# Optimization experiments

Hardware: AMD Instinct MI355X
Metric: run time of the kernel (lower is better)

## Reference

```python
import jax, jax.numpy as jnp
import numpy as np

B, E, N, M = 2, 512, 4096, 4096

def setup_inputs() -> dict:
    key = jax.random.key(0)
    ks = jax.random.split(key, 8)
    s = 1.0 / np.sqrt(E)
    return {
        "src_embedding": jax.random.normal(ks[0], (B, E, N), jnp.float32),
        "tgt_embedding": jax.random.normal(ks[1], (B, E, M), jnp.float32),
        "src": jax.random.normal(ks[2], (B, 3, N), jnp.float32),
        "tgt": jax.random.normal(ks[3], (B, 3, M), jnp.float32),
        "Wq": jax.random.normal(ks[4], (E, E), jnp.float32) * s,
        "bq": jax.random.normal(ks[5], (E,), jnp.float32) * s,
        "Wk": jax.random.normal(ks[6], (E, E), jnp.float32) * s,
        "bk": jax.random.normal(ks[7], (E,), jnp.float32) * s,
    }

def reference(src_embedding, tgt_embedding, src, tgt, Wq, bq, Wk, bk):
    # query/key: [B, N, E] after transpose + Linear (y = x @ W^T + b)
    q = jnp.einsum('ben,fe->bnf', src_embedding, Wq) + bq
    k = jnp.einsum('bem,fe->bmf', tgt_embedding, Wk) + bk
    # pairwise_distance[b,n,m] = -||q_n||^2 + 2 q_n.k_m - ||k_m||^2 = -||q_n - k_m||^2
    inner = jnp.einsum('bne,bme->bnm', q, k)          # [B, N, M]
    qq = jnp.sum(q * q, axis=-1)                      # [B, N]
    kk = jnp.sum(k * k, axis=-1)                      # [B, M]
    pairwise = 2.0 * inner - qq[:, :, None] - kk[:, None, :]
    scores = jax.nn.softmax(pairwise, axis=2)         # softmax over keys (M)
    # src_corr = tgt @ scores^T : [B, 3, N]
    src_corr = jnp.einsum('bdm,bnm->bdn', tgt, scores)
    return (src, src_corr)
```

## Files before the change

kernel.cpp:

```cpp
#include <hip/hip_runtime.h>


typedef _Float16 f16;
typedef __attribute__((ext_vector_type(8))) _Float16 f16x8;
typedef __attribute__((ext_vector_type(4))) float f32x4;

constexpr int B_ = 2, E_ = 512, N_ = 4096, M_ = 4096;
constexpr int MCH = 8;
constexpr float WSCALE = 64.0f;

__device__ __forceinline__ f32x4 mfma16(f16x8 a, f16x8 b, f32x4 c) {
  return __builtin_amdgcn_mfma_f32_16x16x32_f16(a, b, c, 0, 0, 0);
}

__device__ __forceinline__ void gll16(const void* g, void* l) {
  __builtin_amdgcn_global_load_lds(
      (const __attribute__((address_space(1))) unsigned int*)g,
      (__attribute__((address_space(3))) unsigned int*)l, 16, 0, 0);
}


__device__ __forceinline__ void gemm_hl22(
    const f16* __restrict__ AH, const f16* __restrict__ AL,
    const f16* __restrict__ BH, const f16* __restrict__ BL,
    char* lds, f32x4 (&acc)[4][4])
{
  char* ldsA = lds;
  char* ldsB = lds + 16384;
  const int l = threadIdx.x & 63, w = threadIdx.x >> 6;
  const int q = (l & 7) ^ (l >> 3);
  const int rA = w * 8 + (l >> 3);
  const size_t srcoff = (size_t)rA * E_ + (q & 3) * 8;
  const f16* sA = (q < 4 ? AH : AL) + srcoff;
  const f16* sB = (q < 4 ? BH : BL) + srcoff;
  char* dA = ldsA + w * 1024;
  char* dB = ldsB + w * 1024;

  const int r15 = l & 15;
  const int pH16 = ((l >> 4) ^ (l & 7)) * 16;
  const int wr = (w >> 1) * 64, wc = (w & 1) * 64;
  const char* rAh = ldsA + (wr + r15) * 128 + pH16;
  const char* rAl = ldsA + (wr + r15) * 128 + (pH16 ^ 64);
  const char* rBh = ldsB + (wc + r15) * 128 + pH16;
  const char* rBl = ldsB + (wc + r15) * 128 + (pH16 ^ 64);

  for (int e0 = 0; e0 < E_; e0 += 32) {
#pragma unroll
    for (int c = 0; c < 4; ++c) {
      gll16(sA + (size_t)c * 32 * E_, dA + c * 4096);
      gll16(sB + (size_t)c * 32 * E_, dB + c * 4096);
    }
    sA += 32; sB += 32;
    __syncthreads();
    f16x8 ah[4], al[4], bh[4], bl[4];
#pragma unroll
    for (int i = 0; i < 4; ++i) {
      ah[i] = *(const f16x8*)(rAh + i * 2048);
      al[i] = *(const f16x8*)(rAl + i * 2048);
      bh[i] = *(const f16x8*)(rBh + i * 2048);
      bl[i] = *(const f16x8*)(rBl + i * 2048);
    }
#pragma unroll
    for (int i = 0; i < 4; ++i)
#pragma unroll
      for (int j = 0; j < 4; ++j) {
        acc[i][j] = mfma16(ah[i], bh[j], acc[i][j]);
        acc[i][j] = mfma16(ah[i], bl[j], acc[i][j]);
        acc[i][j] = mfma16(al[i], bh[j], acc[i][j]);
      }
    __syncthreads();
  }
}

__device__ __forceinline__ void gemm_hl41(
    const f16* __restrict__ AH, const f16* __restrict__ AL,
    const f16* __restrict__ BH, const f16* __restrict__ BL,
    char* lds, f32x4 (&acc)[2][8])
{
  char* ldsA = lds;
  char* ldsB = lds + 16384;
  const int l = threadIdx.x & 63, w = threadIdx.x >> 6;
  const int q = (l & 7) ^ (l >> 3);
  const int rA = w * 8 + (l >> 3);
  const size_t srcoff = (size_t)rA * E_ + (q & 3) * 8;
  const f16* sA = (q < 4 ? AH : AL) + srcoff;
  const f16* sB = (q < 4 ? BH : BL) + srcoff;
  char* dA = ldsA + w * 1024;
  char* dB = ldsB + w * 1024;

  const int r15 = l & 15;
  const int pH16 = ((l >> 4) ^ (l & 7)) * 16;
  const char* rAh = ldsA + (w * 32 + r15) * 128 + pH16;
  const char* rAl = ldsA + (w * 32 + r15) * 128 + (pH16 ^ 64);
  const char* rBh = ldsB + r15 * 128 + pH16;
  const char* rBl = ldsB + r15 * 128 + (pH16 ^ 64);

  for (int e0 = 0; e0 < E_; e0 += 32) {
#pragma unroll
    for (int c = 0; c < 4; ++c) {
      gll16(sA + (size_t)c * 32 * E_, dA + c * 4096);
      gll16(sB + (size_t)c * 32 * E_, dB + c * 4096);
    }
    sA += 32; sB += 32;
    __syncthreads();
    f16x8 ah0 = *(const f16x8*)(rAh);
    f16x8 ah1 = *(const f16x8*)(rAh + 2048);
    f16x8 al0 = *(const f16x8*)(rAl);
    f16x8 al1 = *(const f16x8*)(rAl + 2048);
#pragma unroll
    for (int j = 0; j < 8; ++j) {
      f16x8 bh = *(const f16x8*)(rBh + j * 2048);
      f16x8 bl = *(const f16x8*)(rBl + j * 2048);
      acc[0][j] = mfma16(ah0, bh, acc[0][j]);
      acc[1][j] = mfma16(ah1, bh, acc[1][j]);
      acc[0][j] = mfma16(ah0, bl, acc[0][j]);
      acc[1][j] = mfma16(ah1, bl, acc[1][j]);
      acc[0][j] = mfma16(al0, bh, acc[0][j]);
      acc[1][j] = mfma16(al1, bh, acc[1][j]);
    }
    __syncthreads();
  }
}

__global__ void k_split_w(const float* __restrict__ Wq, const float* __restrict__ Wk,
                          f16* __restrict__ WqH, f16* __restrict__ WqL,
                          f16* __restrict__ WkH, f16* __restrict__ WkL) {
  int i = blockIdx.x * 256 + threadIdx.x;
  float a = Wq[i] * WSCALE;
  f16 ah = (f16)a; WqH[i] = ah; WqL[i] = (f16)(a - (float)ah);
  float b = Wk[i] * WSCALE;
  f16 bh = (f16)b; WkH[i] = bh; WkL[i] = (f16)(b - (float)bh);
}

__global__ void k_tsplit(const float* __restrict__ Xq, const float* __restrict__ Xk,
                         f16* __restrict__ XqH, f16* __restrict__ XqL,
                         f16* __restrict__ XkH, f16* __restrict__ XkL) {
  __shared__ float tile[64][65];
  const int b = blockIdx.z >> 1, which = blockIdx.z & 1;
  const float* X = (which ? Xk : Xq) + (size_t)b * E_ * N_;
  f16* H = (which ? XkH : XqH) + (size_t)b * N_ * E_;
  f16* L = (which ? XkL : XqL) + (size_t)b * N_ * E_;
  const int e0 = blockIdx.x * 64, n0 = blockIdx.y * 64;
  const int x = threadIdx.x, y = threadIdx.y;
#pragma unroll
  for (int j = 0; j < 16; ++j) {
    int e = y * 16 + j;
    tile[e][x] = X[(size_t)(e0 + e) * N_ + n0 + x];
  }
  __syncthreads();
#pragma unroll
  for (int j = 0; j < 16; ++j) {
    int nl = y * 16 + j;
    float v = tile[x][nl];
    f16 h = (f16)v;
    H[(size_t)(n0 + nl) * E_ + e0 + x] = h;
    L[(size_t)(n0 + nl) * E_ + e0 + x] = (f16)(v - (float)h);
  }
}

__global__ __launch_bounds__(256) void k_proj(
    const f16* __restrict__ XqH, const f16* __restrict__ XqL,
    const f16* __restrict__ XkH, const f16* __restrict__ XkL,
    const f16* __restrict__ WqH, const f16* __restrict__ WqL,
    const f16* __restrict__ WkH, const f16* __restrict__ WkL,
    const float* __restrict__ bq, const float* __restrict__ bk,
    f16* __restrict__ QH, f16* __restrict__ QL,
    f16* __restrict__ KH, f16* __restrict__ KL) {
  __shared__ char lds[32768];
  const int b = blockIdx.z >> 1, kind = blockIdx.z & 1;
  const f16* AH = (kind ? XkH : XqH) + (size_t)b * N_ * E_;
  const f16* AL = (kind ? XkL : XqL) + (size_t)b * N_ * E_;
  const f16* BH = kind ? WkH : WqH;
  const f16* BL = kind ? WkL : WqL;
  const float* bias = kind ? bk : bq;
  f16* OH = (kind ? KH : QH) + (size_t)b * N_ * E_;
  f16* OL = (kind ? KL : QL) + (size_t)b * N_ * E_;
  const int n0 = blockIdx.x * 128, f0 = blockIdx.y * 128;
  const int lane = threadIdx.x & 63, w = threadIdx.x >> 6;
  const int wr = (w >> 1) * 64, wc = (w & 1) * 64;
  const int r15 = lane & 15;

  f32x4 acc[4][4] = {};
  gemm_hl22(AH + (size_t)n0 * E_, AL + (size_t)n0 * E_,
            BH + (size_t)f0 * E_, BL + (size_t)f0 * E_, lds, acc);

  const int rowg = (lane >> 4) * 4;
#pragma unroll
  for (int j = 0; j < 4; ++j) {
    int f = f0 + wc + j * 16 + r15;
    float bv = bias[f];
#pragma unroll
    for (int i = 0; i < 4; ++i) {
#pragma unroll
      for (int r = 0; r < 4; ++r) {
        int n = n0 + wr + i * 16 + rowg + r;
        float qv = acc[i][j][r] * (1.0f / WSCALE) + bv;
        f16 h = (f16)qv;
        OH[(size_t)n * E_ + f] = h;
        OL[(size_t)n * E_ + f] = (f16)(qv - (float)h);
      }
    }
  }
}

__global__ void k_kk(const f16* __restrict__ KH, const f16* __restrict__ KL,
                     float* __restrict__ kk) {
  int row = blockIdx.x * 4 + (threadIdx.x >> 6);
  int lane = threadIdx.x & 63;
  f16x8 h8 = *(const f16x8*)(KH + (size_t)row * E_ + lane * 8);
  f16x8 l8 = *(const f16x8*)(KL + (size_t)row * E_ + lane * 8);
  float s = 0.f;
#pragma unroll
  for (int i = 0; i < 8; ++i) {
    float v = (float)h8[i] + (float)l8[i];
    s += v * v;
  }
#pragma unroll
  for (int o = 32; o; o >>= 1) s += __shfl_xor(s, o);
  if (lane == 0) kk[row] = s;
}

__global__ __launch_bounds__(256, 2) void k_flash(
    const f16* __restrict__ QH, const f16* __restrict__ QL,
    const f16* __restrict__ KH, const f16* __restrict__ KL,
    const float* __restrict__ kk, const float* __restrict__ tgt,
    float* __restrict__ part) {
  __shared__ char lds[40960];
  float* kks = (float*)(lds + 32768);
  float* tgs = (float*)(lds + 34816);
  const int b = blockIdx.z;
  const int n0 = blockIdx.x * 128;
  const int mc = blockIdx.y;
  const int m0c = mc * 512;
  const int tid = threadIdx.x, l = tid & 63, w = tid >> 6;
  const int r15 = l & 15;

  for (int i = tid; i < 512; i += 256) kks[i] = kk[(size_t)b * M_ + m0c + i];
  for (int i = tid; i < 1536; i += 256) {
    int d = i >> 9, m = i & 511;
    tgs[i] = tgt[((size_t)b * 3 + d) * M_ + m0c + m];
  }

  const f16* AH = QH + ((size_t)b * N_ + n0) * E_;
  const f16* AL = QL + ((size_t)b * N_ + n0) * E_;

  float mrun[8], psum[8], pp0[8], pp1[8], pp2[8];
#pragma unroll
  for (int x = 0; x < 8; ++x) {
    mrun[x] = -3.0e38f; psum[x] = 0.f; pp0[x] = 0.f; pp1[x] = 0.f; pp2[x] = 0.f;
  }

  for (int mt = 0; mt < 4; ++mt) {
    const int m0 = m0c + mt * 128;
    const f16* BH = KH + ((size_t)b * M_ + m0) * E_;
    const f16* BL = KL + ((size_t)b * M_ + m0) * E_;
    f32x4 acc[2][8] = {};
    gemm_hl41(AH, AL, BH, BL, lds, acc);

    float kv[8], tv0[8], tv1[8], tv2[8];
#pragma unroll
    for (int j = 0; j < 8; ++j) {
      int ml = mt * 128 + j * 16 + r15;
      kv[j] = kks[ml];
      tv0[j] = tgs[ml];
      tv1[j] = tgs[512 + ml];
      tv2[j] = tgs[1024 + ml];
    }
#pragma unroll
    for (int i = 0; i < 2; ++i) {
#pragma unroll
      for (int r = 0; r < 4; ++r) {
        const int x = i * 4 + r;
        float s[8];
        float rmax = -3.0e38f;
#pragma unroll
        for (int j = 0; j < 8; ++j) {
          s[j] = 2.0f * acc[i][j][r] - kv[j];
          rmax = fmaxf(rmax, s[j]);
        }
        rmax = fmaxf(rmax, __shfl_xor(rmax, 1));
        rmax = fmaxf(rmax, __shfl_xor(rmax, 2));
        rmax = fmaxf(rmax, __shfl_xor(rmax, 4));
        rmax = fmaxf(rmax, __shfl_xor(rmax, 8));
        float nm = fmaxf(mrun[x], rmax);
        float sc = __expf(mrun[x] - nm);
        mrun[x] = nm;
        psum[x] *= sc; pp0[x] *= sc; pp1[x] *= sc; pp2[x] *= sc;
#pragma unroll
        for (int j = 0; j < 8; ++j) {
          float e = __expf(s[j] - nm);
          psum[x] += e;
          pp0[x] += e * tv0[j];
          pp1[x] += e * tv1[j];
          pp2[x] += e * tv2[j];
        }
      }
    }
  }

#pragma unroll
  for (int x = 0; x < 8; ++x) {
#pragma unroll
    for (int o = 1; o <= 8; o <<= 1) {
      psum[x] += __shfl_xor(psum[x], o);
      pp0[x] += __shfl_xor(pp0[x], o);
      pp1[x] += __shfl_xor(pp1[x], o);
      pp2[x] += __shfl_xor(pp2[x], o);
    }
  }
  if (r15 == 0) {
    const int hi = l >> 4;
#pragma unroll
    for (int x = 0; x < 8; ++x) {
      int i = x >> 2, r = x & 3;
      int n = n0 + w * 32 + i * 16 + hi * 4 + r;
      size_t pb = ((size_t)(b * N_ + n) * MCH + mc) * 5;
      part[pb + 0] = mrun[x];
      part[pb + 1] = psum[x];
      part[pb + 2] = pp0[x];
      part[pb + 3] = pp1[x];
      part[pb + 4] = pp2[x];
    }
  }
}

__global__ void k_comb(const float* __restrict__ part, float* __restrict__ out) {
  int idx = blockIdx.x * 256 + threadIdx.x;
  int b = idx >> 12, n = idx & (N_ - 1);
  const float* p = part + (size_t)idx * MCH * 5;
  float M = -3.0e38f;
#pragma unroll
  for (int c = 0; c < MCH; ++c) M = fmaxf(M, p[c * 5]);
  float S = 0.f, P0 = 0.f, P1 = 0.f, P2 = 0.f;
#pragma unroll
  for (int c = 0; c < MCH; ++c) {
    float e = __expf(p[c * 5] - M);
    S += p[c * 5 + 1] * e;
    P0 += p[c * 5 + 2] * e;
    P1 += p[c * 5 + 3] * e;
    P2 += p[c * 5 + 4] * e;
  }
  float inv = 1.0f / S;
  float* oc = out + (size_t)B_ * 3 * N_;
  oc[((size_t)b * 3 + 0) * N_ + n] = P0 * inv;
  oc[((size_t)b * 3 + 1) * N_ + n] = P1 * inv;
  oc[((size_t)b * 3 + 2) * N_ + n] = P2 * inv;
}

__global__ void k_copy(const float* __restrict__ src, float* __restrict__ out) {
  int i = blockIdx.x * 256 + threadIdx.x;
  out[i] = src[i];
}

extern "C" void kernel_launch(void* const* d_in, const int* in_sizes, int n_in,
                              void* d_out, int out_size, void* d_ws, size_t ws_size,
                              hipStream_t stream) {
  const float* src_emb = (const float*)d_in[0];
  const float* tgt_emb = (const float*)d_in[1];
  const float* src     = (const float*)d_in[2];
  const float* tgt     = (const float*)d_in[3];
  const float* Wq      = (const float*)d_in[4];
  const float* bq      = (const float*)d_in[5];
  const float* Wk      = (const float*)d_in[6];
  const float* bk      = (const float*)d_in[7];
  float* out = (float*)d_out;

  constexpr size_t SZX = (size_t)B_ * N_ * E_;
  constexpr size_t OFFW = 4 * SZX * sizeof(f16);
  constexpr size_t OFFQ = OFFW + 4 * (size_t)E_ * E_ * sizeof(f16);
  constexpr size_t OFFK2 = OFFQ + 4 * SZX * sizeof(f16);
  constexpr size_t OFFP = OFFK2 + (size_t)B_ * M_ * sizeof(float);
  constexpr size_t NEED = OFFP + (size_t)B_ * N_ * MCH * 5 * sizeof(float);
  if (ws_size < NEED) return;

  char* ws = (char*)d_ws;
  f16* XqH = (f16*)(ws);
  f16* XqL = XqH + SZX;
  f16* XkH = XqL + SZX;
  f16* XkL = XkH + SZX;
  f16* WqH = (f16*)(ws + OFFW);
  f16* WqL = WqH + (size_t)E_ * E_;
  f16* WkH = WqL + (size_t)E_ * E_;
  f16* WkL = WkH + (size_t)E_ * E_;
  f16* QH = (f16*)(ws + OFFQ);
  f16* QL = QH + SZX;
  f16* KH = QL + SZX;
  f16* KL = KH + SZX;
  float* kk = (float*)(ws + OFFK2);
  float* part = (float*)(ws + OFFP);

  k_split_w<<<dim3(E_ * E_ / 256), 256, 0, stream>>>(Wq, Wk, WqH, WqL, WkH, WkL);
  k_tsplit<<<dim3(E_ / 64, N_ / 64, B_ * 2), dim3(64, 4), 0, stream>>>(
      src_emb, tgt_emb, XqH, XqL, XkH, XkL);
  k_proj<<<dim3(N_ / 128, E_ / 128, B_ * 2), 256, 0, stream>>>(
      XqH, XqL, XkH, XkL, WqH, WqL, WkH, WkL, bq, bk, QH, QL, KH, KL);
  k_kk<<<dim3(B_ * M_ / 4), 256, 0, stream>>>(KH, KL, kk);
  k_flash<<<dim3(N_ / 128, MCH, B_), 256, 0, stream>>>(QH, QL, KH, KL, kk, tgt, part);
  k_comb<<<dim3(B_ * N_ / 256), 256, 0, stream>>>(part, out);
  k_copy<<<dim3(B_ * 3 * N_ / 256), 256, 0, stream>>>(src, out);
}
```

Before: 250.1 us.

## Double-buffer LDS tiles with async prefetch in projection and flash GEMMs

Replaces the single-buffered GEMM helpers with inline double-buffered loops. The next K-slice is issued via global_load_lds while the current one is consumed, with vmcnt waits and raw s_barrier in place of __syncthreads. In the flash kernel the prefetch runs continuously across the M-tile boundaries. It also adds setprio around the MFMA blocks and raises launch bounds for k_proj. LDS use doubles (64KB and 72KB per block), which may limit occupancy. The flash kernel's 72KB may not allow two blocks per CU as its launch bounds request.

```diff
diff --git a/kernel.cpp b/kernel.cpp
--- a/kernel.cpp
+++ b/kernel.cpp
@@ -12,115 +12,14 @@
 __device__ __forceinline__ f32x4 mfma16(f16x8 a, f16x8 b, f32x4 c) {
   return __builtin_amdgcn_mfma_f32_16x16x32_f16(a, b, c, 0, 0, 0);
 }
-
 __device__ __forceinline__ void gll16(const void* g, void* l) {
   __builtin_amdgcn_global_load_lds(
       (const __attribute__((address_space(1))) unsigned int*)g,
       (__attribute__((address_space(3))) unsigned int*)l, 16, 0, 0);
 }
-
-
-__device__ __forceinline__ void gemm_hl22(
-    const f16* __restrict__ AH, const f16* __restrict__ AL,
-    const f16* __restrict__ BH, const f16* __restrict__ BL,
-    char* lds, f32x4 (&acc)[4][4])
-{
-  char* ldsA = lds;
-  char* ldsB = lds + 16384;
-  const int l = threadIdx.x & 63, w = threadIdx.x >> 6;
-  const int q = (l & 7) ^ (l >> 3);
-  const int rA = w * 8 + (l >> 3);
-  const size_t srcoff = (size_t)rA * E_ + (q & 3) * 8;
-  const f16* sA = (q < 4 ? AH : AL) + srcoff;
-  const f16* sB = (q < 4 ? BH : BL) + srcoff;
-  char* dA = ldsA + w * 1024;
-  char* dB = ldsB + w * 1024;
-
-  const int r15 = l & 15;
-  const int pH16 = ((l >> 4) ^ (l & 7)) * 16;
-  const int wr = (w >> 1) * 64, wc = (w & 1) * 64;
-  const char* rAh = ldsA + (wr + r15) * 128 + pH16;
-  const char* rAl = ldsA + (wr + r15) * 128 + (pH16 ^ 64);
-  const char* rBh = ldsB + (wc + r15) * 128 + pH16;
-  const char* rBl = ldsB + (wc + r15) * 128 + (pH16 ^ 64);
-
-  for (int e0 = 0; e0 < E_; e0 += 32) {
-#pragma unroll
-    for (int c = 0; c < 4; ++c) {
-      gll16(sA + (size_t)c * 32 * E_, dA + c * 4096);
-      gll16(sB + (size_t)c * 32 * E_, dB + c * 4096);
-    }
-    sA += 32; sB += 32;
-    __syncthreads();
-    f16x8 ah[4], al[4], bh[4], bl[4];
-#pragma unroll
-    for (int i = 0; i < 4; ++i) {
-      ah[i] = *(const f16x8*)(rAh + i * 2048);
-      al[i] = *(const f16x8*)(rAl + i * 2048);
-      bh[i] = *(const f16x8*)(rBh + i * 2048);
-      bl[i] = *(const f16x8*)(rBl + i * 2048);
-    }
-#pragma unroll
-    for (int i = 0; i < 4; ++i)
-#pragma unroll
-      for (int j = 0; j < 4; ++j) {
-        acc[i][j] = mfma16(ah[i], bh[j], acc[i][j]);
-        acc[i][j] = mfma16(ah[i], bl[j], acc[i][j]);
-        acc[i][j] = mfma16(al[i], bh[j], acc[i][j]);
-      }
-    __syncthreads();
-  }
-}
-
-__device__ __forceinline__ void gemm_hl41(
-    const f16* __restrict__ AH, const f16* __restrict__ AL,
-    const f16* __restrict__ BH, const f16* __restrict__ BL,
-    char* lds, f32x4 (&acc)[2][8])
-{
-  char* ldsA = lds;
-  char* ldsB = lds + 16384;
-  const int l = threadIdx.x & 63, w = threadIdx.x >> 6;
-  const int q = (l & 7) ^ (l >> 3);
-  const int rA = w * 8 + (l >> 3);
-  const size_t srcoff = (size_t)rA * E_ + (q & 3) * 8;
-  const f16* sA = (q < 4 ? AH : AL) + srcoff;
-  const f16* sB = (q < 4 ? BH : BL) + srcoff;
-  char* dA = ldsA + w * 1024;
-  char* dB = ldsB + w * 1024;
-
-  const int r15 = l & 15;
-  const int pH16 = ((l >> 4) ^ (l & 7)) * 16;
-  const char* rAh = ldsA + (w * 32 + r15) * 128 + pH16;
-  const char* rAl = ldsA + (w * 32 + r15) * 128 + (pH16 ^ 64);
-  const char* rBh = ldsB + r15 * 128 + pH16;
-  const char* rBl = ldsB + r15 * 128 + (pH16 ^ 64);
-
-  for (int e0 = 0; e0 < E_; e0 += 32) {
-#pragma unroll
-    for (int c = 0; c < 4; ++c) {
-      gll16(sA + (size_t)c * 32 * E_, dA + c * 4096);
-      gll16(sB + (size_t)c * 32 * E_, dB + c * 4096);
-    }
-    sA += 32; sB += 32;
-    __syncthreads();
-    f16x8 ah0 = *(const f16x8*)(rAh);
-    f16x8 ah1 = *(const f16x8*)(rAh + 2048);
-    f16x8 al0 = *(const f16x8*)(rAl);
-    f16x8 al1 = *(const f16x8*)(rAl + 2048);
-#pragma unroll
-    for (int j = 0; j < 8; ++j) {
-      f16x8 bh = *(const f16x8*)(rBh + j * 2048);
-      f16x8 bl = *(const f16x8*)(rBl + j * 2048);
-      acc[0][j] = mfma16(ah0, bh, acc[0][j]);
-      acc[1][j] = mfma16(ah1, bh, acc[1][j]);
-      acc[0][j] = mfma16(ah0, bl, acc[0][j]);
-      acc[1][j] = mfma16(ah1, bl, acc[1][j]);
-      acc[0][j] = mfma16(al0, bh, acc[0][j]);
-      acc[1][j] = mfma16(al1, bh, acc[1][j]);
-    }
-    __syncthreads();
-  }
-}
+__device__ __forceinline__ void waitv8() { asm volatile("s_waitcnt vmcnt(8)" ::: "memory"); }
+__device__ __forceinline__ void waitv0() { asm volatile("s_waitcnt vmcnt(0)" ::: "memory"); }
+
 
 __global__ void k_split_w(const float* __restrict__ Wq, const float* __restrict__ Wk,
                           f16* __restrict__ WqH, f16* __restrict__ WqL,
@@ -158,7 +57,7 @@
   }
 }
 
-__global__ __launch_bounds__(256) void k_proj(
+__global__ __launch_bounds__(256, 2) void k_proj(
     const f16* __restrict__ XqH, const f16* __restrict__ XqL,
     const f16* __restrict__ XkH, const f16* __restrict__ XkL,
     const f16* __restrict__ WqH, const f16* __restrict__ WqL,
@@ -166,7 +65,7 @@
     const float* __restrict__ bq, const float* __restrict__ bk,
     f16* __restrict__ QH, f16* __restrict__ QL,
     f16* __restrict__ KH, f16* __restrict__ KL) {
-  __shared__ char lds[32768];
+  __shared__ char lds[65536];
   const int b = blockIdx.z >> 1, kind = blockIdx.z & 1;
   const f16* AH = (kind ? XkH : XqH) + (size_t)b * N_ * E_;
   const f16* AL = (kind ? XkL : XqL) + (size_t)b * N_ * E_;
@@ -176,15 +75,62 @@
   f16* OH = (kind ? KH : QH) + (size_t)b * N_ * E_;
   f16* OL = (kind ? KL : QL) + (size_t)b * N_ * E_;
   const int n0 = blockIdx.x * 128, f0 = blockIdx.y * 128;
-  const int lane = threadIdx.x & 63, w = threadIdx.x >> 6;
+  const int l = threadIdx.x & 63, w = threadIdx.x >> 6;
   const int wr = (w >> 1) * 64, wc = (w & 1) * 64;
-  const int r15 = lane & 15;
+  const int r15 = l & 15;
+
+  const int q = (l & 7) ^ (l >> 3);
+  const size_t soff = (size_t)(w * 8 + (l >> 3)) * E_ + (q & 3) * 8;
+  const f16* sA = (q < 4 ? AH : AL) + (size_t)n0 * E_ + soff;
+  const f16* sB = (q < 4 ? BH : BL) + (size_t)f0 * E_ + soff;
+
+  auto STAGE = [&](int k) {
+    char* dA = lds + ((k & 1) << 14) + w * 1024;
+    char* dB = lds + 32768 + ((k & 1) << 14) + w * 1024;
+    const f16* pa = sA + k * 32;
+    const f16* pb = sB + k * 32;
+#pragma unroll
+    for (int c = 0; c < 4; ++c) {
+      gll16(pa + (size_t)c * 32 * E_, dA + c * 4096);
+      gll16(pb + (size_t)c * 32 * E_, dB + c * 4096);
+    }
+  };
+
+  const int pH16 = ((l >> 4) ^ (l & 7)) * 16;
+  const int aoffH = (wr + r15) * 128 + pH16;
+  const int boffH = (wc + r15) * 128 + pH16;
 
   f32x4 acc[4][4] = {};
-  gemm_hl22(AH + (size_t)n0 * E_, AL + (size_t)n0 * E_,
-            BH + (size_t)f0 * E_, BL + (size_t)f0 * E_, lds, acc);
-
-  const int rowg = (lane >> 4) * 4;
+  STAGE(0);
+#pragma unroll 2
+  for (int k = 0; k < 16; ++k) {
+    if (k < 15) { STAGE(k + 1); waitv8(); } else { waitv0(); }
+    __builtin_amdgcn_sched_barrier(0);
+    __builtin_amdgcn_s_barrier();
+    const char* cA = lds + ((k & 1) << 14);
+    const char* cB = lds + 32768 + ((k & 1) << 14);
+    f16x8 ah[4], al[4], bh[4], bl[4];
+#pragma unroll
+    for (int i = 0; i < 4; ++i) {
+      ah[i] = *(const f16x8*)(cA + aoffH + i * 2048);
+      al[i] = *(const f16x8*)(cA + (aoffH ^ 64) + i * 2048);
+      bh[i] = *(const f16x8*)(cB + boffH + i * 2048);
+      bl[i] = *(const f16x8*)(cB + (boffH ^ 64) + i * 2048);
+    }
+    __builtin_amdgcn_s_setprio(1);
+#pragma unroll
+    for (int i = 0; i < 4; ++i)
+#pragma unroll
+      for (int j = 0; j < 4; ++j) {
+        acc[i][j] = mfma16(ah[i], bh[j], acc[i][j]);
+        acc[i][j] = mfma16(ah[i], bl[j], acc[i][j]);
+        acc[i][j] = mfma16(al[i], bh[j], acc[i][j]);
+      }
+    __builtin_amdgcn_s_setprio(0);
+    __builtin_amdgcn_s_barrier();
+  }
+
+  const int rowg = (l >> 4) * 4;
 #pragma unroll
   for (int j = 0; j < 4; ++j) {
     int f = f0 + wc + j * 16 + r15;
@@ -225,13 +171,12 @@
     const f16* __restrict__ KH, const f16* __restrict__ KL,
     const float* __restrict__ kk, const float* __restrict__ tgt,
     float* __restrict__ part) {
-  __shared__ char lds[40960];
-  float* kks = (float*)(lds + 32768);
-  float* tgs = (float*)(lds + 34816);
+  __shared__ char lds[73728];
+  float* kks = (float*)(lds + 65536);
+  float* tgs = (float*)(lds + 67584);
   const int b = blockIdx.z;
   const int n0 = blockIdx.x * 128;
-  const int mc = blockIdx.y;
-  const int m0c = mc * 512;
+  const int mc = blockIdx.y, m0c = mc * 512;
   const int tid = threadIdx.x, l = tid & 63, w = tid >> 6;
   const int r15 = l & 15;
 
@@ -243,6 +188,30 @@
 
   const f16* AH = QH + ((size_t)b * N_ + n0) * E_;
   const f16* AL = QL + ((size_t)b * N_ + n0) * E_;
+  const f16* BHb = KH + ((size_t)b * M_ + m0c) * E_;
+  const f16* BLb = KL + ((size_t)b * M_ + m0c) * E_;
+
+  const int q = (l & 7) ^ (l >> 3);
+  const size_t soff = (size_t)(w * 8 + (l >> 3)) * E_ + (q & 3) * 8;
+  const f16* sA = (q < 4 ? AH : AL) + soff;
+  const f16* sB = (q < 4 ? BHb : BLb) + soff;
+
+  auto STAGE = [&](int s) {
+    int mt_ = s >> 4, k_ = s & 15;
+    char* dA = lds + ((s & 1) << 14) + w * 1024;
+    char* dB = lds + 32768 + ((s & 1) << 14) + w * 1024;
+    const f16* pa = sA + k_ * 32;
+    const f16* pb = sB + (size_t)mt_ * 128 * E_ + k_ * 32;
+#pragma unroll
+    for (int c = 0; c < 4; ++c) {
+      gll16(pa + (size_t)c * 32 * E_, dA + c * 4096);
+      gll16(pb + (size_t)c * 32 * E_, dB + c * 4096);
+    }
+  };
+
+  const int pH16 = ((l >> 4) ^ (l & 7)) * 16;
+  const int aoffH = (w * 32 + r15) * 128 + pH16;
+  const int boffH = r15 * 128 + pH16;
 
   float mrun[8], psum[8], pp0[8], pp1[8], pp2[8];
 #pragma unroll
@@ -250,12 +219,36 @@
     mrun[x] = -3.0e38f; psum[x] = 0.f; pp0[x] = 0.f; pp1[x] = 0.f; pp2[x] = 0.f;
   }
 
+  STAGE(0);
   for (int mt = 0; mt < 4; ++mt) {
-    const int m0 = m0c + mt * 128;
-    const f16* BH = KH + ((size_t)b * M_ + m0) * E_;
-    const f16* BL = KL + ((size_t)b * M_ + m0) * E_;
     f32x4 acc[2][8] = {};
-    gemm_hl41(AH, AL, BH, BL, lds, acc);
+#pragma unroll 2
+    for (int k = 0; k < 16; ++k) {
+      const int s = mt * 16 + k;
+      if (s < 63) { STAGE(s + 1); waitv8(); } else { waitv0(); }
+      __builtin_amdgcn_sched_barrier(0);
+      __builtin_amdgcn_s_barrier();
+      const char* cA = lds + ((s & 1) << 14);
+      const char* cB = lds + 32768 + ((s & 1) << 14);
+      f16x8 ah0 = *(const f16x8*)(cA + aoffH);
+      f16x8 ah1 = *(const f16x8*)(cA + aoffH + 2048);
+      f16x8 al0 = *(const f16x8*)(cA + (aoffH ^ 64));
+      f16x8 al1 = *(const f16x8*)(cA + (aoffH ^ 64) + 2048);
+      __builtin_amdgcn_s_setprio(1);
+#pragma unroll
+      for (int j = 0; j < 8; ++j) {
+        f16x8 bh = *(const f16x8*)(cB + boffH + j * 2048);
+        f16x8 bl = *(const f16x8*)(cB + (boffH ^ 64) + j * 2048);
+        acc[0][j] = mfma16(ah0, bh, acc[0][j]);
+        acc[1][j] = mfma16(ah1, bh, acc[1][j]);
+        acc[0][j] = mfma16(ah0, bl, acc[0][j]);
+        acc[1][j] = mfma16(ah1, bl, acc[1][j]);
+        acc[0][j] = mfma16(al0, bh, acc[0][j]);
+        acc[1][j] = mfma16(al1, bh, acc[1][j]);
+      }
+      __builtin_amdgcn_s_setprio(0);
+      __builtin_amdgcn_s_barrier();
+    }
 
     float kv[8], tv0[8], tv1[8], tv2[8];
 #pragma unroll
```

Result: faster. 237.9 us (-4.9%).
